# Kernel tuning notes

Measured on AMD Instinct MI355X. Metric: run time of the kernel, lower is better.

The kernel has to match this reference:

```python
import jax, jax.numpy as jnp
import numpy as np

N = 50000  # num nodes
E = 800000  # num edges


def gcn_layer(x, W, b, senders, receivers, snorm, rnorm):
    # jraph.GraphConvolution(Dense, add_self_edges=False, symmetric_normalization=True)
    h = x @ W + b                       # [N, F_out] dense transform
    h = h * snorm[:, None]              # scale by rsqrt(max(sender_degree, 1))
    agg = jax.ops.segment_sum(h[senders], receivers, num_segments=N)  # scatter-add over edges
    return agg * rnorm[:, None]         # scale by rsqrt(max(receiver_degree, 1))


def setup_inputs() -> dict:
    key = jax.random.key(0)
    ks = jax.random.split(key, 6)
    nodes = jax.random.normal(ks[0], (N, 128), jnp.float32)
    senders = jax.random.randint(ks[1], (E,), 0, N)
    receivers = jax.random.randint(ks[2], (E,), 0, N)

    def dense(k, fin, fout):
        kw, _ = jax.random.split(k)
        scale = 1.0 / np.sqrt(fin).astype(np.float32)
        W = jax.random.uniform(kw, (fin, fout), jnp.float32, -scale, scale)
        b = jnp.zeros((fout,), jnp.float32)
        return W, b

    W1, b1 = dense(ks[3], 128, 256)
    W2, b2 = dense(ks[4], 256, 256)
    W3, b3 = dense(ks[5], 256, 128)
    return dict(nodes=nodes, senders=senders, receivers=receivers,
                W1=W1, b1=b1, W2=W2, b2=b2, W3=W3, b3=b3)


def reference(nodes, senders, receivers, W1, b1, W2, b2, W3, b3):
    ones = jnp.ones((E,), nodes.dtype)
    sdeg = jax.ops.segment_sum(ones, senders, num_segments=N)
    rdeg = jax.ops.segment_sum(ones, receivers, num_segments=N)
    snorm = jax.lax.rsqrt(jnp.maximum(sdeg, 1.0))
    rnorm = jax.lax.rsqrt(jnp.maximum(rdeg, 1.0))

    x = nodes
    for W, b in ((W1, b1), (W2, b2), (W3, b3)):
        x = gcn_layer(x, W, b, senders, receivers, snorm, rnorm)
        x = jax.nn.relu(x)  # activation applied after every layer, incl. last
        # dropout is deterministic (eval mode) -> identity
    return x
```

## Files before the change

### kernel.cpp

```cpp
#include <hip/hip_runtime.h>
#include <hip/hip_fp16.h>


typedef __attribute__((ext_vector_type(8))) short short8;
typedef __attribute__((ext_vector_type(4))) float f32x4;

#define DCAP 64
#define PBITS 8
#define EPB 4096

static __device__ __forceinline__ float reluf(float x){ return x > 0.f ? x : 0.f; }

static __device__ __forceinline__ unsigned short bf16_rn(float v){
    unsigned u = __float_as_uint(v);
    unsigned r = u + 0x7FFFu + ((u >> 16) & 1u);
    return (unsigned short)(r >> 16);
}
static __device__ __forceinline__ void split2(float v, unsigned short& h, unsigned short& l){
    unsigned short hh = bf16_rn(v);
    float hf = __uint_as_float(((unsigned)hh) << 16);
    h = hh;
    l = bf16_rn(v - hf);
}
static __device__ __forceinline__ unsigned short f2h(float v){
    return __half_as_ushort(__float2half(v));
}
static __device__ __forceinline__ float h2f(unsigned short u){
    return __half2float(__ushort_as_half(u));
}

static __device__ __forceinline__ void gload_lds16(const void* g, void* lds){
    __builtin_amdgcn_global_load_lds((const __attribute__((address_space(1))) unsigned int*)g,
                                     (__attribute__((address_space(3))) unsigned int*)lds, 16, 0, 0);
}


__global__ __launch_bounds__(256)
void p1_hist(const int* __restrict__ snd, const int* __restrict__ rcv,
             int* __restrict__ cntR, int* __restrict__ cntS, int e, int NP, int NB)
{
    __shared__ int hR[256], hS[256];
    int t = threadIdx.x;
    hR[t] = 0; hS[t] = 0;
    __syncthreads();
    int base = blockIdx.x * EPB;
#pragma unroll
    for (int k = 0; k < EPB / 256; ++k) {
        int i = base + k * 256 + t;
        if (i < e) {
            atomicAdd(&hR[rcv[i] >> PBITS], 1);
            atomicAdd(&hS[snd[i] >> PBITS], 1);
        }
    }
    __syncthreads();
    if (t < NP) {
        cntR[t * NB + blockIdx.x] = hR[t];
        cntS[t * NB + blockIdx.x] = hS[t];
    }
}

__global__ __launch_bounds__(256)
void p2a_scanpart(const int* __restrict__ cntR, int* __restrict__ withinR, int* __restrict__ totR,
                  const int* __restrict__ cntS, int* __restrict__ withinS, int* __restrict__ totS,
                  int NB)
{
    __shared__ int s[256];
    int t = threadIdx.x;
    int p = blockIdx.x;
    int v = (t < NB) ? cntR[p * NB + t] : 0;
    s[t] = v;
    __syncthreads();
    for (int d = 1; d < 256; d <<= 1) {
        int x = (t >= d) ? s[t - d] : 0;
        __syncthreads();
        s[t] += x;
        __syncthreads();
    }
    if (t < NB) withinR[p * NB + t] = s[t] - v;
    if (t == 255) totR[p] = s[255];
    __syncthreads();
    v = (t < NB) ? cntS[p * NB + t] : 0;
    s[t] = v;
    __syncthreads();
    for (int d = 1; d < 256; d <<= 1) {
        int x = (t >= d) ? s[t - d] : 0;
        __syncthreads();
        s[t] += x;
        __syncthreads();
    }
    if (t < NB) withinS[p * NB + t] = s[t] - v;
    if (t == 255) totS[p] = s[255];
}

__global__ __launch_bounds__(256)
void p2b_scantops(const int* __restrict__ totR, int* __restrict__ pbaseR,
                  const int* __restrict__ totS, int* __restrict__ pbaseS, int NP)
{
    __shared__ int s[256];
    int t = threadIdx.x;
    int v = (t < NP) ? totR[t] : 0;
    s[t] = v;
    __syncthreads();
    for (int d = 1; d < 256; d <<= 1) {
        int x = (t >= d) ? s[t - d] : 0;
        __syncthreads();
        s[t] += x;
        __syncthreads();
    }
    if (t < NP) pbaseR[t] = s[t] - v;
    if (t == 255) pbaseR[NP] = s[255];
    __syncthreads();
    v = (t < NP) ? totS[t] : 0;
    s[t] = v;
    __syncthreads();
    for (int d = 1; d < 256; d <<= 1) {
        int x = (t >= d) ? s[t - d] : 0;
        __syncthreads();
        s[t] += x;
        __syncthreads();
    }
    if (t < NP) pbaseS[t] = s[t] - v;
    if (t == 255) pbaseS[NP] = s[255];
}

__global__ __launch_bounds__(256)
void p3_scatter(const int* __restrict__ snd, const int* __restrict__ rcv,
                const int* __restrict__ pbaseR, const int* __restrict__ withinR,
                const int* __restrict__ pbaseS, const int* __restrict__ withinS,
                unsigned int* __restrict__ eP, unsigned short* __restrict__ sP,
                int e, int NP, int NB)
{
    __shared__ int bR[256], cR[256], bS[256], cS[256];
    int t = threadIdx.x;
    if (t < NP) {
        bR[t] = pbaseR[t] + withinR[t * NB + blockIdx.x];
        bS[t] = pbaseS[t] + withinS[t * NB + blockIdx.x];
    }
    cR[t] = 0; cS[t] = 0;
    __syncthreads();
    int base = blockIdx.x * EPB;
#pragma unroll
    for (int k = 0; k < EPB / 256; ++k) {
        int i = base + k * 256 + t;
        if (i < e) {
            int s = snd[i], r = rcv[i];
            int pr = r >> PBITS, ps = s >> PBITS;
            int rk = atomicAdd(&cR[pr], 1);
            eP[bR[pr] + rk] = ((unsigned)r << 16) | (unsigned)s;
            int sk = atomicAdd(&cS[ps], 1);
            sP[bS[ps] + sk] = (unsigned short)s;
        }
    }
}

__global__ __launch_bounds__(256)
void p4_csr(const unsigned int* __restrict__ eP, const int* __restrict__ pbaseR,
            unsigned short* __restrict__ esrc, int* __restrict__ rcnt,
            float* __restrict__ rnorm, int n)
{
    __shared__ unsigned short buck[256 * DCAP];
    __shared__ int cnt[256];
    int t = threadIdx.x;
    cnt[t] = 0;
    for (int k = t; k < 256 * DCAP; k += 256) buck[k] = 0;
    __syncthreads();
    int p = blockIdx.x;
    int lo = pbaseR[p];
    int hi = pbaseR[p + 1];
    for (int i = lo + t; i < hi; i += 256) {
        unsigned u = eP[i];
        int lr = (u >> 16) & 255;
        int slot = atomicAdd(&cnt[lr], 1);
        if (slot < DCAP) buck[lr * DCAP + slot] = (unsigned short)(u & 0xFFFFu);
    }
    __syncthreads();
    int g = p * 256 + t;
    if (g < n) {
        int full = cnt[t];
        rcnt[g] = min(full, DCAP);
        rnorm[g] = rsqrtf(fmaxf((float)full, 1.0f));
        unsigned short* dst = esrc + (size_t)g * DCAP;
        const unsigned short* src = buck + t * DCAP;
#pragma unroll
        for (int k = 0; k < DCAP / 8; ++k)
            *(short8*)(dst + k * 8) = *(const short8*)(src + k * 8);
    }
}

__global__ __launch_bounds__(256)
void p4b_sdeg(const unsigned short* __restrict__ sP, const int* __restrict__ pbaseS,
              float* __restrict__ snorm, int n)
{
    __shared__ int cnt[256];
    int t = threadIdx.x;
    cnt[t] = 0;
    __syncthreads();
    int p = blockIdx.x;
    int lo = pbaseS[p];
    int hi = pbaseS[p + 1];
    for (int i = lo + t; i < hi; i += 256)
        atomicAdd(&cnt[sP[i] & 255], 1);
    __syncthreads();
    int g = p * 256 + t;
    if (g < n) snorm[g] = rsqrtf(fmaxf((float)cnt[t], 1.0f));
}

__global__ void conv_h_kernel(const float* __restrict__ x, unsigned short* __restrict__ y, int total4)
{
    int i = blockIdx.x * 256 + threadIdx.x;
    if (i >= total4) return;
    float4 v = *(const float4*)(x + (size_t)i * 4);
    ushort4 o = make_ushort4(f2h(v.x), f2h(v.y), f2h(v.z), f2h(v.w));
    *(ushort4*)(y + (size_t)i * 4) = o;
}

__global__ void wsplit_kernel(const float* __restrict__ W, unsigned short* __restrict__ Th,
                              unsigned short* __restrict__ Tl, int K, int N)
{
    int i = blockIdx.x * 256 + threadIdx.x;
    if (i >= K * N) return;
    int k = i / N, c = i % N;
    unsigned short h, l;
    split2(W[i], h, l);
    Th[c * K + k] = h;
    Tl[c * K + k] = l;
}

template<int K, int NOUT, int OMODE, bool APAIR>
__global__ __launch_bounds__(256)
void mfma_gemm(const unsigned short* __restrict__ A_g,
               const unsigned short* __restrict__ Bh_g, const unsigned short* __restrict__ Bl_g,
               const float* __restrict__ bias, const float* __restrict__ rs,
               const float* __restrict__ bs, float* __restrict__ Ht,
               unsigned short* __restrict__ Ot, int n)
{
    __shared__ unsigned short smem[4 * 128 * 32];
    unsigned short* Ah = smem;
    unsigned short* Al = smem + 4096;
    unsigned short* Bh = smem + 8192;
    unsigned short* Bl = smem + 12288;

    const int tid = threadIdx.x;
    const int wid = tid >> 6, lane = tid & 63;
    const int wr = (wid >> 1) * 64, wc = (wid & 1) * 64;
    const int r0 = blockIdx.x * 128, c0 = blockIdx.y * 128;

    f32x4 acc[4][4];
#pragma unroll
    for (int m = 0; m < 4; ++m)
#pragma unroll
        for (int q = 0; q < 4; ++q) acc[m][q] = (f32x4){0.f, 0.f, 0.f, 0.f};

    const int ks = lane >> 4, lr = lane & 15;
    const int ASTRIDE = APAIR ? 2 * K : K;

    for (int k0 = 0; k0 < K; k0 += 32) {
#pragma unroll
        for (int c = 0; c < 2; ++c) {
            int i = tid + c * 256;
            int row = i >> 2, p = i & 3;
            int g = p ^ ((row >> 1) & 3);
            int ar = r0 + row; if (ar >= n) ar = n - 1;
            size_t aoff = (size_t)ar * ASTRIDE + k0 + g * 8;
            gload_lds16(A_g + aoff, Ah + i * 8);
            if (APAIR) gload_lds16(A_g + aoff + K, Al + i * 8);
            size_t boff = (size_t)(c0 + row) * K + k0 + g * 8;
            gload_lds16(Bh_g + boff, Bh + i * 8);
            gload_lds16(Bl_g + boff, Bl + i * 8);
        }
        __syncthreads();

        short8 a_h[4], a_l[4], b_h[4], b_l[4];
#pragma unroll
        for (int m = 0; m < 4; ++m) {
            int r = wr + m * 16 + lr;
            int slot = ks ^ ((r >> 1) & 3);
            a_h[m] = *(const short8*)(Ah + r * 32 + slot * 8);
            if (APAIR) a_l[m] = *(const short8*)(Al + r * 32 + slot * 8);
        }
#pragma unroll
        for (int q = 0; q < 4; ++q) {
            int r = wc + q * 16 + lr;
            int slot = ks ^ ((r >> 1) & 3);
            b_h[q] = *(const short8*)(Bh + r * 32 + slot * 8);
            b_l[q] = *(const short8*)(Bl + r * 32 + slot * 8);
        }
#pragma unroll
        for (int m = 0; m < 4; ++m)
#pragma unroll
            for (int q = 0; q < 4; ++q) {
                acc[m][q] = __builtin_amdgcn_mfma_f32_16x16x32_bf16(a_h[m], b_h[q], acc[m][q], 0, 0, 0);
                acc[m][q] = __builtin_amdgcn_mfma_f32_16x16x32_bf16(a_h[m], b_l[q], acc[m][q], 0, 0, 0);
                if (APAIR)
                    acc[m][q] = __builtin_amdgcn_mfma_f32_16x16x32_bf16(a_l[m], b_h[q], acc[m][q], 0, 0, 0);
            }
        __syncthreads();
    }

    const int lq = lane >> 4;
    float* eps = (float*)smem;
    unsigned short* eph = smem;
    unsigned short* epl = smem + 32 * 136;

#pragma unroll
    for (int m = 0; m < 4; ++m) {
        __syncthreads();
#pragma unroll
        for (int j = 0; j < 4; ++j) {
            int gr = r0 + wr + m * 16 + lq * 4 + j;
            int cr = (wid >> 1) * 16 + lq * 4 + j;
            float rsv, bsv;
            if (gr < n) { rsv = rs[gr]; bsv = bs[gr]; } else { rsv = 0.f; bsv = 0.f; }
#pragma unroll
            for (int q = 0; q < 4; ++q) {
                int col = wc + q * 16 + lr;
                float v = acc[m][q][j] * rsv + bias[c0 + col] * bsv;
                if (OMODE == 1) {
                    v = reluf(v);
                    unsigned short h, l;
                    split2(v, h, l);
                    eph[cr * 136 + col] = h;
                    epl[cr * 136 + col] = l;
                } else if (OMODE == 2) {
                    eph[cr * 136 + col] = f2h(v);
                } else if (OMODE == 3) {
                    eph[cr * 136 + col] = bf16_rn(reluf(v));
                } else {
                    eps[cr * 132 + col] = v;
                }
            }
        }
        __syncthreads();
        int rr = tid >> 3, seg = tid & 7;
        int gr = r0 + (rr >> 4) * 64 + m * 16 + (rr & 15);
        if (gr < n) {
            if (OMODE == 1) {
                unsigned short* dst = Ot + (size_t)gr * (2 * NOUT) + c0 + seg * 16;
#pragma unroll
                for (int k = 0; k < 2; ++k) {
                    *(short8*)(dst + k * 8) = *(const short8*)(eph + rr * 136 + seg * 16 + k * 8);
                    *(short8*)(dst + NOUT + k * 8) = *(const short8*)(epl + rr * 136 + seg * 16 + k * 8);
                }
            } else if (OMODE == 2 || OMODE == 3) {
                unsigned short* dst = Ot + (size_t)gr * NOUT + c0 + seg * 16;
#pragma unroll
                for (int k = 0; k < 2; ++k)
                    *(short8*)(dst + k * 8) = *(const short8*)(eph + rr * 136 + seg * 16 + k * 8);
            } else {
                float* dst = Ht + (size_t)gr * NOUT + c0 + seg * 16;
#pragma unroll
                for (int k = 0; k < 4; ++k)
                    *(float4*)(dst + k * 4) = *(const float4*)(eps + rr * 132 + seg * 16 + k * 4);
            }
        }
    }
}


__global__ __launch_bounds__(256)
void gather1_t(const unsigned short* __restrict__ Nh, const int* __restrict__ rcnt,
               const unsigned short* __restrict__ esrc, const float* __restrict__ snorm,
               const float* __restrict__ rnorm,
               unsigned short* __restrict__ G, float* __restrict__ bs, int n)
{
    int g = blockIdx.x * 256 + threadIdx.x;
    int node = g >> 4, lane = g & 15;
    if (node >= n) return;
    int col = blockIdx.y * 64 + lane * 4;
    const unsigned short* Nc = Nh + col;
    int e0 = node * DCAP;
    int e1 = e0 + rcnt[node];
    float a0 = 0, a1 = 0, a2 = 0, a3 = 0, gs = 0;
    int e = e0;
    for (; e + 4 <= e1; e += 4) {
        int s0 = esrc[e], s1 = esrc[e + 1], s2 = esrc[e + 2], s3 = esrc[e + 3];
        float n0 = snorm[s0], n1 = snorm[s1], n2 = snorm[s2], n3 = snorm[s3];
        ushort4 v0 = *(const ushort4*)(Nc + (size_t)s0 * 128);
        ushort4 v1 = *(const ushort4*)(Nc + (size_t)s1 * 128);
        ushort4 v2 = *(const ushort4*)(Nc + (size_t)s2 * 128);
        ushort4 v3 = *(const ushort4*)(Nc + (size_t)s3 * 128);
        a0 += h2f(v0.x) * n0 + h2f(v1.x) * n1 + h2f(v2.x) * n2 + h2f(v3.x) * n3;
        a1 += h2f(v0.y) * n0 + h2f(v1.y) * n1 + h2f(v2.y) * n2 + h2f(v3.y) * n3;
        a2 += h2f(v0.z) * n0 + h2f(v1.z) * n1 + h2f(v2.z) * n2 + h2f(v3.z) * n3;
        a3 += h2f(v0.w) * n0 + h2f(v1.w) * n1 + h2f(v2.w) * n2 + h2f(v3.w) * n3;
        gs += n0 + n1 + n2 + n3;
    }
    for (; e < e1; ++e) {
        int s = esrc[e];
        float ns = snorm[s];
        ushort4 v = *(const ushort4*)(Nc + (size_t)s * 128);
        a0 += h2f(v.x) * ns; a1 += h2f(v.y) * ns; a2 += h2f(v.z) * ns; a3 += h2f(v.w) * ns;
        gs += ns;
    }
    unsigned short h[4], l[4];
    float vv[4] = { a0, a1, a2, a3 };
#pragma unroll
    for (int i = 0; i < 4; ++i) split2(vv[i], h[i], l[i]);
    size_t o = (size_t)node * 256 + col;
    *(ushort4*)(G + o) = make_ushort4(h[0], h[1], h[2], h[3]);
    *(ushort4*)(G + o + 128) = make_ushort4(l[0], l[1], l[2], l[3]);
    if (blockIdx.y == 0 && lane == 0) bs[node] = gs * rnorm[node];
}

__global__ __launch_bounds__(256)
void gather2_t(const unsigned short* __restrict__ Hh, const int* __restrict__ rcnt,
               const unsigned short* __restrict__ esrc, const float* __restrict__ rnorm,
               unsigned short* __restrict__ X3, int n)
{
    int g = blockIdx.x * 256 + threadIdx.x;
    int node = g >> 4, lane = g & 15;
    if (node >= n) return;
    int col = blockIdx.y * 64 + lane * 4;
    const unsigned short* Hc = Hh + col;
    int e0 = node * DCAP;
    int e1 = e0 + rcnt[node];
    float a0 = 0, a1 = 0, a2 = 0, a3 = 0;
    int e = e0;
    for (; e + 4 <= e1; e += 4) {
        int s0 = esrc[e], s1 = esrc[e + 1], s2 = esrc[e + 2], s3 = esrc[e + 3];
        ushort4 v0 = *(const ushort4*)(Hc + (size_t)s0 * 256);
        ushort4 v1 = *(const ushort4*)(Hc + (size_t)s1 * 256);
        ushort4 v2 = *(const ushort4*)(Hc + (size_t)s2 * 256);
        ushort4 v3 = *(const ushort4*)(Hc + (size_t)s3 * 256);
        a0 += h2f(v0.x) + h2f(v1.x) + h2f(v2.x) + h2f(v3.x);
        a1 += h2f(v0.y) + h2f(v1.y) + h2f(v2.y) + h2f(v3.y);
        a2 += h2f(v0.z) + h2f(v1.z) + h2f(v2.z) + h2f(v3.z);
        a3 += h2f(v0.w) + h2f(v1.w) + h2f(v2.w) + h2f(v3.w);
    }
    for (; e < e1; ++e) {
        int s = esrc[e];
        ushort4 v = *(const ushort4*)(Hc + (size_t)s * 256);
        a0 += h2f(v.x); a1 += h2f(v.y); a2 += h2f(v.z); a3 += h2f(v.w);
    }
    float rn = rnorm[node];
    ushort4 o = make_ushort4(bf16_rn(reluf(a0 * rn)), bf16_rn(reluf(a1 * rn)),
                             bf16_rn(reluf(a2 * rn)), bf16_rn(reluf(a3 * rn)));
    *(ushort4*)(X3 + (size_t)node * 256 + col) = o;
}

__global__ __launch_bounds__(256)
void gather3_t(const unsigned short* __restrict__ Hh, const int* __restrict__ rcnt,
               const unsigned short* __restrict__ esrc, const float* __restrict__ rnorm,
               float* __restrict__ out, int n)
{
    int g = blockIdx.x * 256 + threadIdx.x;
    int node = g >> 4, lane = g & 15;
    if (node >= n) return;
    int col = blockIdx.y * 64 + lane * 4;
    const unsigned short* Hc = Hh + col;
    int e0 = node * DCAP;
    int e1 = e0 + rcnt[node];
    float a0 = 0, a1 = 0, a2 = 0, a3 = 0;
    int e = e0;
    for (; e + 4 <= e1; e += 4) {
        int s0 = esrc[e], s1 = esrc[e + 1], s2 = esrc[e + 2], s3 = esrc[e + 3];
        ushort4 v0 = *(const ushort4*)(Hc + (size_t)s0 * 128);
        ushort4 v1 = *(const ushort4*)(Hc + (size_t)s1 * 128);
        ushort4 v2 = *(const ushort4*)(Hc + (size_t)s2 * 128);
        ushort4 v3 = *(const ushort4*)(Hc + (size_t)s3 * 128);
        a0 += h2f(v0.x) + h2f(v1.x) + h2f(v2.x) + h2f(v3.x);
        a1 += h2f(v0.y) + h2f(v1.y) + h2f(v2.y) + h2f(v3.y);
        a2 += h2f(v0.z) + h2f(v1.z) + h2f(v2.z) + h2f(v3.z);
        a3 += h2f(v0.w) + h2f(v1.w) + h2f(v2.w) + h2f(v3.w);
    }
    for (; e < e1; ++e) {
        int s = esrc[e];
        ushort4 v = *(const ushort4*)(Hc + (size_t)s * 128);
        a0 += h2f(v.x); a1 += h2f(v.y); a2 += h2f(v.z); a3 += h2f(v.w);
    }
    float rn = rnorm[node];
    float4 o = { reluf(a0 * rn), reluf(a1 * rn), reluf(a2 * rn), reluf(a3 * rn) };
    *(float4*)(out + (size_t)node * 128 + col) = o;
}


extern "C" void kernel_launch(void* const* d_in, const int* in_sizes, int n_in,
                              void* d_out, int out_size, void* d_ws, size_t ws_size,
                              hipStream_t stream)
{
    const float* nodes = (const float*)d_in[0];
    const int*   snd   = (const int*)d_in[1];
    const int*   rcv   = (const int*)d_in[2];
    const float* W1    = (const float*)d_in[3];
    const float* b1    = (const float*)d_in[4];
    const float* W2    = (const float*)d_in[5];
    const float* b2    = (const float*)d_in[6];
    const float* W3    = (const float*)d_in[7];
    const float* b3    = (const float*)d_in[8];
    const int n = in_sizes[0] / 128;
    const int e = in_sizes[1];
    float* out = (float*)d_out;

    const int NP = (n + 255) >> 8;
    const int NB = (e + EPB - 1) / EPB;

    char* w = (char*)d_ws;
    size_t o = 0;
    auto alloc = [&](size_t b){ size_t p = o; o += (b + 255) & ~(size_t)255; return p; };
    unsigned short* Hh   = (unsigned short*)(w + alloc((size_t)n * 256 * 2));
    unsigned short* X2   = (unsigned short*)(w + alloc((size_t)n * 256 * 2));
    char*           bufA = w + alloc((size_t)n * 512 * 2);
    unsigned short* Nh   = (unsigned short*)bufA;
    unsigned short* G    = (unsigned short*)(bufA + (size_t)n * 128 * 2);
    unsigned short* X3   = (unsigned short*)bufA;
    unsigned short* Wt1h = (unsigned short*)(w + alloc(256 * 128 * 2));
    unsigned short* Wt1l = (unsigned short*)(w + alloc(256 * 128 * 2));
    unsigned short* Wt2h = (unsigned short*)(w + alloc(256 * 256 * 2));
    unsigned short* Wt2l = (unsigned short*)(w + alloc(256 * 256 * 2));
    unsigned short* Wt3h = (unsigned short*)(w + alloc(128 * 256 * 2));
    unsigned short* Wt3l = (unsigned short*)(w + alloc(128 * 256 * 2));
    float* bsb   = (float*)(w + alloc((size_t)n * 4));
    int*   cntR   = (int*)(w + alloc((size_t)NP * NB * 4));
    int*   withinR= (int*)(w + alloc((size_t)NP * NB * 4));
    int*   cntS   = (int*)(w + alloc((size_t)NP * NB * 4));
    int*   withinS= (int*)(w + alloc((size_t)NP * NB * 4));
    int*   totR   = (int*)(w + alloc((size_t)NP * 4));
    int*   totS   = (int*)(w + alloc((size_t)NP * 4));
    int*   pbaseR = (int*)(w + alloc((size_t)(NP + 1) * 4));
    int*   pbaseS = (int*)(w + alloc((size_t)(NP + 1) * 4));
    unsigned int*   eP   = (unsigned int*)  (w + alloc((size_t)e * 4));
    unsigned short* sP   = (unsigned short*)(w + alloc((size_t)e * 2));
    unsigned short* esrc = (unsigned short*)(w + alloc((size_t)n * DCAP * 2));
    int*   rcnt  = (int*)  (w + alloc((size_t)n * 4));
    float* snorm = (float*)(w + alloc((size_t)n * 4));
    float* rnorm = (float*)(w + alloc((size_t)n * 4));

    p1_hist<<<NB, 256, 0, stream>>>(snd, rcv, cntR, cntS, e, NP, NB);
    p2a_scanpart<<<NP, 256, 0, stream>>>(cntR, withinR, totR, cntS, withinS, totS, NB);
    p2b_scantops<<<1, 256, 0, stream>>>(totR, pbaseR, totS, pbaseS, NP);
    p3_scatter<<<NB, 256, 0, stream>>>(snd, rcv, pbaseR, withinR, pbaseS, withinS, eP, sP, e, NP, NB);
    p4_csr<<<NP, 256, 0, stream>>>(eP, pbaseR, esrc, rcnt, rnorm, n);
    p4b_sdeg<<<NP, 256, 0, stream>>>(sP, pbaseS, snorm, n);

    conv_h_kernel<<<((size_t)n * 32 + 255) / 256, 256, 0, stream>>>(nodes, Nh, n * 32);
    wsplit_kernel<<<(128 * 256 + 255) / 256, 256, 0, stream>>>(W1, Wt1h, Wt1l, 128, 256);
    wsplit_kernel<<<(256 * 256 + 255) / 256, 256, 0, stream>>>(W2, Wt2h, Wt2l, 256, 256);
    wsplit_kernel<<<(256 * 128 + 255) / 256, 256, 0, stream>>>(W3, Wt3h, Wt3l, 256, 128);

    int gb = (n + 127) / 128;
    int lb = ((size_t)n * 16 + 255) / 256;

    gather1_t<<<dim3(lb, 2), 256, 0, stream>>>(Nh, rcnt, esrc, snorm, rnorm, G, bsb, n);
    mfma_gemm<128, 256, 3, true><<<dim3(gb, 2), 256, 0, stream>>>(G, Wt1h, Wt1l, b1, rnorm, bsb,
                                                                  (float*)nullptr, X2, n);
    mfma_gemm<256, 256, 2, false><<<dim3(gb, 2), 256, 0, stream>>>(X2, Wt2h, Wt2l, b2, snorm, snorm,
                                                                   (float*)nullptr, Hh, n);
    gather2_t<<<dim3(lb, 4), 256, 0, stream>>>(Hh, rcnt, esrc, rnorm, X3, n);
    mfma_gemm<256, 128, 2, false><<<dim3(gb, 1), 256, 0, stream>>>(X3, Wt3h, Wt3l, b3, snorm, snorm,
                                                                   (float*)nullptr, Hh, n);
    gather3_t<<<dim3(lb, 2), 256, 0, stream>>>(Hh, rcnt, esrc, rnorm, out, n);
}
```

Before: 263.2 us.

## Renumber nodes by in-degree within partitions and drop layer-1 split precision

Within each 256-node partition, receiver nodes are sorted by clamped in-degree. Every node-indexed array (features, esrc, norms) is permuted into that order, and an inverse map is applied to edge sources and to the final output. The goal is to cut wavefront divergence in the gather loops, since neighbouring nodes then have similar edge counts. The first gather also stops writing the hi/lo bf16 split and emits only the hi part, with the GEMM APAIR flag disabled, which halves G traffic but lowers the precision of layer 1. It also removes the zero-fill of the shared bucket and adds one remap kernel.

```diff
diff --git a/kernel.cpp b/kernel.cpp
--- a/kernel.cpp
+++ b/kernel.cpp
@@ -155,14 +155,15 @@
 
 __global__ __launch_bounds__(256)
 void p4_csr(const unsigned int* __restrict__ eP, const int* __restrict__ pbaseR,
-            unsigned short* __restrict__ esrc, int* __restrict__ rcnt,
-            float* __restrict__ rnorm, int n)
+            unsigned short* __restrict__ esrc, int* __restrict__ rcntP,
+            float* __restrict__ rnormP, int* __restrict__ inv, int n)
 {
     __shared__ unsigned short buck[256 * DCAP];
     __shared__ int cnt[256];
+    __shared__ int hist[64], hbase[64], cur[64], sc[64];
     int t = threadIdx.x;
     cnt[t] = 0;
-    for (int k = t; k < 256 * DCAP; k += 256) buck[k] = 0;
+    if (t < 64) { hist[t] = 0; cur[t] = 0; }
     __syncthreads();
     int p = blockIdx.x;
     int lo = pbaseR[p];
@@ -174,12 +175,28 @@
         if (slot < DCAP) buck[lr * DCAP + slot] = (unsigned short)(u & 0xFFFFu);
     }
     __syncthreads();
-    int g = p * 256 + t;
-    if (g < n) {
+    int nvalid = min(256, n - p * 256);
+    int deg = (t < nvalid) ? min(cnt[t], 63) : -1;
+    if (deg >= 0) atomicAdd(&hist[deg], 1);
+    __syncthreads();
+    int hv = (t < 64) ? hist[t] : 0;
+    if (t < 64) sc[t] = hv;
+    __syncthreads();
+    for (int d = 1; d < 64; d <<= 1) {
+        int x = (t < 64 && t >= d) ? sc[t - d] : 0;
+        __syncthreads();
+        if (t < 64) sc[t] += x;
+        __syncthreads();
+    }
+    if (t < 64) hbase[t] = sc[t] - hv;
+    __syncthreads();
+    if (deg >= 0) {
+        int slot = p * 256 + hbase[deg] + atomicAdd(&cur[deg], 1);
+        inv[p * 256 + t] = slot;
         int full = cnt[t];
-        rcnt[g] = min(full, DCAP);
-        rnorm[g] = rsqrtf(fmaxf((float)full, 1.0f));
-        unsigned short* dst = esrc + (size_t)g * DCAP;
+        rcntP[slot] = min(full, DCAP);
+        rnormP[slot] = rsqrtf(fmaxf((float)full, 1.0f));
+        unsigned short* dst = esrc + (size_t)slot * DCAP;
         const unsigned short* src = buck + t * DCAP;
 #pragma unroll
         for (int k = 0; k < DCAP / 8; ++k)
@@ -189,7 +206,7 @@
 
 __global__ __launch_bounds__(256)
 void p4b_sdeg(const unsigned short* __restrict__ sP, const int* __restrict__ pbaseS,
-              float* __restrict__ snorm, int n)
+              float* __restrict__ snormN, int n)
 {
     __shared__ int cnt[256];
     int t = threadIdx.x;
@@ -202,16 +219,31 @@
         atomicAdd(&cnt[sP[i] & 255], 1);
     __syncthreads();
     int g = p * 256 + t;
-    if (g < n) snorm[g] = rsqrtf(fmaxf((float)cnt[t], 1.0f));
-}
-
-__global__ void conv_h_kernel(const float* __restrict__ x, unsigned short* __restrict__ y, int total4)
+    if (g < n) snormN[g] = rsqrtf(fmaxf((float)cnt[t], 1.0f));
+}
+
+__global__ __launch_bounds__(256)
+void p5_remap(unsigned short* __restrict__ esrc, const int* __restrict__ rcntP,
+              const int* __restrict__ inv, const float* __restrict__ snormN,
+              float* __restrict__ snormP, int n)
 {
     int i = blockIdx.x * 256 + threadIdx.x;
-    if (i >= total4) return;
-    float4 v = *(const float4*)(x + (size_t)i * 4);
+    if (i < n) snormP[inv[i]] = snormN[i];
+    if (i < n * DCAP) {
+        int slot = i >> 6, j = i & 63;
+        if (j < rcntP[slot]) esrc[i] = (unsigned short)inv[esrc[i]];
+    }
+}
+
+__global__ void conv_h_kernel(const float* __restrict__ x, unsigned short* __restrict__ y,
+                              const int* __restrict__ inv, int n)
+{
+    int i = blockIdx.x * 256 + threadIdx.x;
+    if (i >= n * 32) return;
+    int node = i >> 5, c4 = i & 31;
+    float4 v = *(const float4*)(x + (size_t)node * 128 + c4 * 4);
     ushort4 o = make_ushort4(f2h(v.x), f2h(v.y), f2h(v.z), f2h(v.w));
-    *(ushort4*)(y + (size_t)i * 4) = o;
+    *(ushort4*)(y + (size_t)inv[node] * 128 + c4 * 4) = o;
 }
 
 __global__ void wsplit_kernel(const float* __restrict__ W, unsigned short* __restrict__ Th,
@@ -358,9 +390,9 @@
 
 
 __global__ __launch_bounds__(256)
-void gather1_t(const unsigned short* __restrict__ Nh, const int* __restrict__ rcnt,
-               const unsigned short* __restrict__ esrc, const float* __restrict__ snorm,
-               const float* __restrict__ rnorm,
+void gather1_t(const unsigned short* __restrict__ Nh, const int* __restrict__ rcntP,
+               const unsigned short* __restrict__ esrc, const float* __restrict__ snormP,
+               const float* __restrict__ rnormP,
                unsigned short* __restrict__ G, float* __restrict__ bs, int n)
 {
     int g = blockIdx.x * 256 + threadIdx.x;
@@ -369,12 +401,12 @@
     int col = blockIdx.y * 64 + lane * 4;
     const unsigned short* Nc = Nh + col;
     int e0 = node * DCAP;
-    int e1 = e0 + rcnt[node];
+    int e1 = e0 + rcntP[node];
     float a0 = 0, a1 = 0, a2 = 0, a3 = 0, gs = 0;
     int e = e0;
     for (; e + 4 <= e1; e += 4) {
         int s0 = esrc[e], s1 = esrc[e + 1], s2 = esrc[e + 2], s3 = esrc[e + 3];
-        float n0 = snorm[s0], n1 = snorm[s1], n2 = snorm[s2], n3 = snorm[s3];
+        float n0 = snormP[s0], n1 = snormP[s1], n2 = snormP[s2], n3 = snormP[s3];
         ushort4 v0 = *(const ushort4*)(Nc + (size_t)s0 * 128);
         ushort4 v1 = *(const ushort4*)(Nc + (size_t)s1 * 128);
         ushort4 v2 = *(const ushort4*)(Nc + (size_t)s2 * 128);
@@ -387,24 +419,19 @@
     }
     for (; e < e1; ++e) {
         int s = esrc[e];
-        float ns = snorm[s];
+        float ns = snormP[s];
         ushort4 v = *(const ushort4*)(Nc + (size_t)s * 128);
         a0 += h2f(v.x) * ns; a1 += h2f(v.y) * ns; a2 += h2f(v.z) * ns; a3 += h2f(v.w) * ns;
         gs += ns;
     }
-    unsigned short h[4], l[4];
-    float vv[4] = { a0, a1, a2, a3 };
-#pragma unroll
-    for (int i = 0; i < 4; ++i) split2(vv[i], h[i], l[i]);
-    size_t o = (size_t)node * 256 + col;
-    *(ushort4*)(G + o) = make_ushort4(h[0], h[1], h[2], h[3]);
-    *(ushort4*)(G + o + 128) = make_ushort4(l[0], l[1], l[2], l[3]);
-    if (blockIdx.y == 0 && lane == 0) bs[node] = gs * rnorm[node];
-}
-
-__global__ __launch_bounds__(256)
-void gather2_t(const unsigned short* __restrict__ Hh, const int* __restrict__ rcnt,
-               const unsigned short* __restrict__ esrc, const float* __restrict__ rnorm,
+    ushort4 o = make_ushort4(bf16_rn(a0), bf16_rn(a1), bf16_rn(a2), bf16_rn(a3));
+    *(ushort4*)(G + (size_t)node * 128 + col) = o;
+    if (blockIdx.y == 0 && lane == 0) bs[node] = gs * rnormP[node];
+}
+
+__global__ __launch_bounds__(256)
+void gather2_t(const unsigned short* __restrict__ Hh, const int* __restrict__ rcntP,
+               const unsigned short* __restrict__ esrc, const float* __restrict__ rnormP,
                unsigned short* __restrict__ X3, int n)
 {
     int g = blockIdx.x * 256 + threadIdx.x;
@@ -413,7 +440,7 @@
     int col = blockIdx.y * 64 + lane * 4;
     const unsigned short* Hc = Hh + col;
     int e0 = node * DCAP;
-    int e1 = e0 + rcnt[node];
+    int e1 = e0 + rcntP[node];
     float a0 = 0, a1 = 0, a2 = 0, a3 = 0;
     int e = e0;
     for (; e + 4 <= e1; e += 4) {
@@ -432,24 +459,25 @@
         ushort4 v = *(const ushort4*)(Hc + (size_t)s * 256);
         a0 += h2f(v.x); a1 += h2f(v.y); a2 += h2f(v.z); a3 += h2f(v.w);
     }
-    float rn = rnorm[node];
+    float rn = rnormP[node];
     ushort4 o = make_ushort4(bf16_rn(reluf(a0 * rn)), bf16_rn(reluf(a1 * rn)),
                              bf16_rn(reluf(a2 * rn)), bf16_rn(reluf(a3 * rn)));
     *(ushort4*)(X3 + (size_t)node * 256 + col) = o;
 }
 
 __global__ __launch_bounds__(256)
-void gather3_t(const unsigned short* __restrict__ Hh, const int* __restrict__ rcnt,
-               const unsigned short* __restrict__ esrc, const float* __restrict__ rnorm,
-               float* __restrict__ out, int n)
+void gather3_t(const unsigned short* __restrict__ Hh, const int* __restrict__ rcntP,
+               const unsigned short* __restrict__ esrc, const float* __restrict__ rnormP,
+               const int* __restrict__ inv, float* __restrict__ out, int n)
 {
     int g = blockIdx.x * 256 + threadIdx.x;
     int node = g >> 4, lane = g & 15;
     if (node >= n) return;
+    int iv = inv[node];
     int col = blockIdx.y * 64 + lane * 4;
     const unsigned short* Hc = Hh + col;
-    int e0 = node * DCAP;
-    int e1 = e0 + rcnt[node];
+    int e0 = iv * DCAP;
+    int e1 = e0 + rcntP[iv];
     float a0 = 0, a1 = 0, a2 = 0, a3 = 0;
     int e = e0;
     for (; e + 4 <= e1; e += 4) {
@@ -468,7 +496,7 @@
         ushort4 v = *(const ushort4*)(Hc + (size_t)s * 128);
         a0 += h2f(v.x); a1 += h2f(v.y); a2 += h2f(v.z); a3 += h2f(v.w);
     }
-    float rn = rnorm[node];
+    float rn = rnormP[iv];
     float4 o = { reluf(a0 * rn), reluf(a1 * rn), reluf(a2 * rn), reluf(a3 * rn) };
     *(float4*)(out + (size_t)node * 128 + col) = o;
 }
@@ -521,18 +549,21 @@
     unsigned int*   eP   = (unsigned int*)  (w + alloc((size_t)e * 4));
     unsigned short* sP   = (unsigned short*)(w + alloc((size_t)e * 2));
     unsigned short* esrc = (unsigned short*)(w + alloc((size_t)n * DCAP * 2));
-    int*   rcnt  = (int*)  (w + alloc((size_t)n * 4));
-    float* snorm = (float*)(w + alloc((size_t)n * 4));
-    float* rnorm = (float*)(w + alloc((size_t)n * 4));
+    int*   rcntP = (int*)  (w + alloc((size_t)n * 4));
+    int*   inv   = (int*)  (w + alloc((size_t)n * 4));
+    float* snormN= (float*)(w + alloc((size_t)n * 4));
+    float* snormP= (float*)(w + alloc((size_t)n * 4));
+    float* rnormP= (float*)(w + alloc((size_t)n * 4));
 
     p1_hist<<<NB, 256, 0, stream>>>(snd, rcv, cntR, cntS, e, NP, NB);
     p2a_scanpart<<<NP, 256, 0, stream>>>(cntR, withinR, totR, cntS, withinS, totS, NB);
     p2b_scantops<<<1, 256, 0, stream>>>(totR, pbaseR, totS, pbaseS, NP);
     p3_scatter<<<NB, 256, 0, stream>>>(snd, rcv, pbaseR, withinR, pbaseS, withinS, eP, sP, e, NP, NB);
-    p4_csr<<<NP, 256, 0, stream>>>(eP, pbaseR, esrc, rcnt, rnorm, n);
-    p4b_sdeg<<<NP, 256, 0, stream>>>(sP, pbaseS, snorm, n);
-
-    conv_h_kernel<<<((size_t)n * 32 + 255) / 256, 256, 0, stream>>>(nodes, Nh, n * 32);
+    p4_csr<<<NP, 256, 0, stream>>>(eP, pbaseR, esrc, rcntP, rnormP, inv, n);
+    p4b_sdeg<<<NP, 256, 0, stream>>>(sP, pbaseS, snormN, n);
+    p5_remap<<<((size_t)n * DCAP + 255) / 256, 256, 0, stream>>>(esrc, rcntP, inv, snormN, snormP, n);
+
+    conv_h_kernel<<<((size_t)n * 32 + 255) / 256, 256, 0, stream>>>(nodes, Nh, inv, n);
     wsplit_kernel<<<(128 * 256 + 255) / 256, 256, 0, stream>>>(W1, Wt1h, Wt1l, 128, 256);
     wsplit_kernel<<<(256 * 256 + 255) / 256, 256, 0, stream>>>(W2, Wt2h, Wt2l, 256, 256);
     wsplit_kernel<<<(256 * 128 + 255) / 256, 256, 0, stream>>>(W3, Wt3h, Wt3l, 256, 128);
@@ -540,13 +571,13 @@
     int gb = (n + 127) / 128;
     int lb = ((size_t)n * 16 + 255) / 256;
 
-    gather1_t<<<dim3(lb, 2), 256, 0, stream>>>(Nh, rcnt, esrc, snorm, rnorm, G, bsb, n);
-    mfma_gemm<128, 256, 3, true><<<dim3(gb, 2), 256, 0, stream>>>(G, Wt1h, Wt1l, b1, rnorm, bsb,
-                                                                  (float*)nullptr, X2, n);
-    mfma_gemm<256, 256, 2, false><<<dim3(gb, 2), 256, 0, stream>>>(X2, Wt2h, Wt2l, b2, snorm, snorm,
+    gather1_t<<<dim3(lb, 2), 256, 0, stream>>>(Nh, rcntP, esrc, snormP, rnormP, G, bsb, n);
+    mfma_gemm<128, 256, 3, false><<<dim3(gb, 2), 256, 0, stream>>>(G, Wt1h, Wt1l, b1, rnormP, bsb,
+                                                                   (float*)nullptr, X2, n);
+    mfma_gemm<256, 256, 2, false><<<dim3(gb, 2), 256, 0, stream>>>(X2, Wt2h, Wt2l, b2, snormP, snormP,
                                                                    (float*)nullptr, Hh, n);
-    gather2_t<<<dim3(lb, 4), 256, 0, stream>>>(Hh, rcnt, esrc, rnorm, X3, n);
-    mfma_gemm<256, 128, 2, false><<<dim3(gb, 1), 256, 0, stream>>>(X3, Wt3h, Wt3l, b3, snorm, snorm,
+    gather2_t<<<dim3(lb, 4), 256, 0, stream>>>(Hh, rcntP, esrc, rnormP, X3, n);
+    mfma_gemm<256, 128, 2, false><<<dim3(gb, 1), 256, 0, stream>>>(X3, Wt3h, Wt3l, b3, snormP, snormP,
                                                                    (float*)nullptr, Hh, n);
-    gather3_t<<<dim3(lb, 2), 256, 0, stream>>>(Hh, rcnt, esrc, rnorm, out, n);
-}
+    gather3_t<<<dim3(lb, 2), 256, 0, stream>>>(Hh, rcntP, esrc, rnormP, inv, out, n);
+}
```

Result: no change. 267.0 us (+1.4%).
